# Optimization experiments

Measured on AMD Instinct MI355X. Metric: run time of the kernel, lower is better.

## Reference

```python
import jax, jax.numpy as jnp
import numpy as np
import math

EMBED_DIM = 256
NUM_HEADS = 8
FFN_DIM = 1024
EPS = 1e-5


def layer_norm(x, g, b):
    mu = jnp.mean(x, axis=-1, keepdims=True)
    var = jnp.var(x, axis=-1, keepdims=True)
    return (x - mu) / jnp.sqrt(var + EPS) * g + b


def setup_inputs() -> dict:
    key = jax.random.key(0)
    ks = jax.random.split(key, 10)
    B, L, D, F = 4, 2048, EMBED_DIM, FFN_DIM
    x = jax.random.normal(ks[0], (B, L, D), dtype=jnp.float32)
    mask = jnp.ones((B, L), dtype=jnp.int32)
    # FFN params (PyTorch Linear default-ish scale)
    W1 = jax.random.normal(ks[1], (D, F), dtype=jnp.float32) / np.sqrt(D)
    b1 = jnp.zeros((F,), dtype=jnp.float32)
    W2 = jax.random.normal(ks[2], (F, D), dtype=jnp.float32) / np.sqrt(F)
    b2 = jnp.zeros((D,), dtype=jnp.float32)
    g1 = jnp.ones((D,), dtype=jnp.float32)
    be1 = jnp.zeros((D,), dtype=jnp.float32)
    g2 = jnp.ones((D,), dtype=jnp.float32)
    be2 = jnp.zeros((D,), dtype=jnp.float32)
    return {"x": x, "mask": mask, "W1": W1, "b1": b1, "W2": W2, "b2": b2,
            "g1": g1, "be1": be1, "g2": g2, "be2": be2}


def quantum_attention(x, mask):
    B, L, D = x.shape
    H, dk = NUM_HEADS, D // NUM_HEADS
    xh = x.reshape(B, L, H, dk).transpose(0, 2, 1, 3)  # [B,H,L,dk]
    # per-token mean over batch and heads -> [L, dk]
    m = jnp.mean(xh, axis=(0, 1))
    # closed form of the single-qubit RX circuit: P(|1>) = sin^2(angle/2)
    dot = m @ m.T  # [L, L]
    ang = jnp.clip(dot, -math.pi, math.pi)
    scores = jnp.sin(ang * 0.5) ** 2  # [L, L], shared across B and H
    attn = jnp.broadcast_to(scores[None, None], (B, H, L, L))
    attn = jnp.where(mask[:, None, None, :] == 0, -1e9, attn)
    attn = jax.nn.softmax(attn, axis=-1)
    out = jnp.einsum('bhij,bhjd->bhid', attn, xh)  # values are xh itself
    return out.transpose(0, 2, 1, 3).reshape(B, L, D)


def reference(x, mask, W1, b1, W2, b2, g1, be1, g2, be2):
    attn_out = quantum_attention(x, mask)
    h = layer_norm(x + attn_out, g1, be1)
    ffn = jax.nn.relu(h @ W1 + b1) @ W2 + b2
    return layer_norm(h + ffn, g2, be2)
```

## Files before the change

### kernel.cpp

```cpp
#include <hip/hip_runtime.h>
#include <hip/hip_bf16.h>


#define B_ 4
#define L_ 2048
#define D_ 256
#define F_ 1024
#define PI_F 3.14159265358979323846f

typedef __bf16 bf16x8 __attribute__((ext_vector_type(8)));
typedef float floatx4 __attribute__((ext_vector_type(4)));

__device__ __forceinline__ unsigned short f2bf(float f) {
    unsigned int u = __float_as_uint(f);
    u = (u + 0x7FFFu + ((u >> 16) & 1u)) >> 16;
    return (unsigned short)u;
}
__device__ __forceinline__ float bf2f(unsigned short u) {
    union { unsigned int i; float f; } v; v.i = ((unsigned int)u) << 16; return v.f;
}

__device__ __forceinline__ void async_cp16(unsigned short* lds, const unsigned short* g) {
    __builtin_amdgcn_global_load_lds(
        (const __attribute__((address_space(1))) unsigned int*)g,
        (__attribute__((address_space(3))) unsigned int*)lds, 16, 0, 0);
}

__global__ __launch_bounds__(256) void k_prep(const float* __restrict__ x,
                                              const float* __restrict__ W1,
                                              const float* __restrict__ W2,
                                              const int* __restrict__ mask,
                                              unsigned short* __restrict__ mb,
                                              unsigned short* __restrict__ XmT,
                                              unsigned short* __restrict__ W1T,
                                              unsigned short* __restrict__ W2T) {
    __shared__ float tile[32][33];
    int r = blockIdx.x, t = threadIdx.x;
    if (r >= 2560) {
        if (r < 2816) {
            int idx = (r - 2560) * 256 + t;
            int l = idx >> 5, k = idx & 31;
            float s = 0.f;
#pragma unroll
            for (int b = 0; b < B_; b++) {
                const float* xp = x + ((size_t)(b * L_ + l)) * D_ + k;
#pragma unroll
                for (int h = 0; h < 8; h++) s += xp[h * 32];
            }
            mb[idx] = f2bf(s * (1.f / 32.f));
        } else {
#pragma unroll
            for (int c = 0; c < 32; c++) {
                int e = c * 256 + t;
                int b = e >> 11, j = e & (L_ - 1);
                XmT[(size_t)(1024 + b) * L_ + j] = mask[b * L_ + j] ? 0x3F80 : 0;
            }
        }
        return;
    }
    const float* in; unsigned short* outp; int R, C; const int* mrow = nullptr; size_t bo = 0;
    int bx, by;
    if (r < 2048) {
        int z = r >> 9, rem = r & 511; by = rem >> 3; bx = rem & 7;
        in = x; outp = XmT; R = L_; C = 256; bo = (size_t)z * R * C; mrow = mask + z * L_;
    } else if (r < 2304) {
        int rem = r - 2048; bx = rem & 31; by = rem >> 5;
        in = W1; outp = W1T; R = 256; C = 1024;
    } else {
        int rem = r - 2304; bx = rem & 7; by = rem >> 3;
        in = W2; outp = W2T; R = 1024; C = 256;
    }
    int r0 = by * 32, c0 = bx * 32;
    int tx = t & 31, ty = t >> 5;
#pragma unroll
    for (int rr = 0; rr < 4; rr++) {
        int rw = ty + rr * 8;
        tile[rw][tx] = in[bo + (size_t)(r0 + rw) * C + c0 + tx];
    }
    float mfac = 1.f;
    if (mrow) mfac = mrow[r0 + tx] ? 1.f : 0.f;
    __syncthreads();
#pragma unroll
    for (int rr = 0; rr < 4; rr++) {
        int c = ty + rr * 8;
        outp[bo + (size_t)(c0 + c) * R + r0 + tx] = f2bf(tile[tx][c] * mfac);
    }
}

__global__ __launch_bounds__(256) void k_scores_mfma(const unsigned short* __restrict__ mb,
                                                     unsigned short* __restrict__ E) {
    const int t = threadIdx.x, lane = t & 63, wid = t >> 6;
    const int wm = (wid >> 1) * 64, wn = (wid & 1) * 32;
    const int lr = lane & 15, lq = lane >> 4;
    int m0 = blockIdx.y * 128, n0 = blockIdx.x * 64;
    bf16x8 af[4], bfr[2];
#pragma unroll
    for (int i = 0; i < 4; i++)
        af[i] = *(const bf16x8*)(mb + (size_t)(m0 + wm + i * 16 + lr) * 32 + lq * 8);
#pragma unroll
    for (int j = 0; j < 2; j++)
        bfr[j] = *(const bf16x8*)(mb + (size_t)(n0 + wn + j * 16 + lr) * 32 + lq * 8);
    floatx4 acc[4][2];
#pragma unroll
    for (int i = 0; i < 4; i++)
#pragma unroll
        for (int j = 0; j < 2; j++) {
            acc[i][j] = (floatx4){0.f, 0.f, 0.f, 0.f};
            acc[i][j] = __builtin_amdgcn_mfma_f32_16x16x32_bf16(af[i], bfr[j], acc[i][j], 0, 0, 0);
        }
#pragma unroll
    for (int i = 0; i < 4; i++)
#pragma unroll
        for (int j = 0; j < 2; j++)
#pragma unroll
            for (int r = 0; r < 4; r++) {
                int row = m0 + wm + i * 16 + lq * 4 + r;
                int col = n0 + wn + j * 16 + lr;
                float d = fminf(fmaxf(acc[i][j][r], -PI_F), PI_F);
                float sn = __sinf(0.5f * d);
                E[(size_t)row * L_ + col] = f2bf(__expf(sn * sn));
            }
}

__device__ __forceinline__ void mfma_gemm_async(const unsigned short* __restrict__ A,
                                                const unsigned short* __restrict__ Bt,
                                                int K, int m0, int n0,
                                                unsigned short* sA, unsigned short* sB,
                                                floatx4 acc[4][2]) {
    const int t = threadIdx.x;
    const int lane = t & 63, wid = t >> 6;
    const int wm = (wid >> 1) * 64, wn = (wid & 1) * 32;
    const int lr = lane & 15, lq = lane >> 4;
    const int lrow = lane >> 3, lseg = lane & 7;

    const unsigned short* Ag[4]; unsigned short* sAd[4];
#pragma unroll
    for (int q = 0; q < 4; q++) {
        int rl = wid * 32 + q * 8 + lrow;
        int seg = (lseg - rl) & 7;
        Ag[q] = A + (size_t)(m0 + rl) * K + seg * 8;
        sAd[q] = sA + (wid * 32 + q * 8) * 64;
    }
    const unsigned short* Bg[2]; unsigned short* sBd[2];
#pragma unroll
    for (int q = 0; q < 2; q++) {
        int rl = wid * 16 + q * 8 + lrow;
        int seg = (lseg - rl) & 7;
        Bg[q] = Bt + (size_t)(n0 + rl) * K + seg * 8;
        sBd[q] = sB + (wid * 16 + q * 8) * 64;
    }
    int arot[4], brot[2];
    const unsigned short* sAr[4]; const unsigned short* sBr[2];
#pragma unroll
    for (int i = 0; i < 4; i++) { int ar = wm + i * 16 + lr; sAr[i] = sA + ar * 64; arot[i] = lq + ar; }
#pragma unroll
    for (int j = 0; j < 2; j++) { int br = wn + j * 16 + lr; sBr[j] = sB + br * 64; brot[j] = lq + br; }

    for (int k0 = 0; k0 < K; k0 += 64) {
        __syncthreads();
#pragma unroll
        for (int q = 0; q < 4; q++) async_cp16(sAd[q], Ag[q] + k0);
#pragma unroll
        for (int q = 0; q < 2; q++) async_cp16(sBd[q], Bg[q] + k0);
        __syncthreads();
#pragma unroll
        for (int s = 0; s < 2; s++) {
            bf16x8 af[4], bfr[2];
#pragma unroll
            for (int i = 0; i < 4; i++)
                af[i] = *(const bf16x8*)(sAr[i] + ((s * 4 + arot[i]) & 7) * 8);
#pragma unroll
            for (int j = 0; j < 2; j++)
                bfr[j] = *(const bf16x8*)(sBr[j] + ((s * 4 + brot[j]) & 7) * 8);
#pragma unroll
            for (int i = 0; i < 4; i++)
#pragma unroll
                for (int j = 0; j < 2; j++)
                    acc[i][j] = __builtin_amdgcn_mfma_f32_16x16x32_bf16(af[i], bfr[j], acc[i][j], 0, 0, 0);
        }
    }
}

__global__ __launch_bounds__(256) void k_av(const unsigned short* __restrict__ E,
                                            const unsigned short* __restrict__ XmT,
                                            unsigned short* __restrict__ Cb) {
    __shared__ __align__(16) unsigned short sA[128 * 64];
    __shared__ __align__(16) unsigned short sB[64 * 64];
    floatx4 acc[4][2];
#pragma unroll
    for (int i = 0; i < 4; i++)
#pragma unroll
        for (int j = 0; j < 2; j++) acc[i][j] = (floatx4){0.f, 0.f, 0.f, 0.f};
    int m0 = blockIdx.y * 128, n0 = blockIdx.x * 64;
    mfma_gemm_async(E, XmT, L_, m0, n0, sA, sB, acc);
    const int lane = threadIdx.x & 63, wid = threadIdx.x >> 6;
    const int wm = (wid >> 1) * 64, wn = (wid & 1) * 32;
    const int lr = lane & 15, lq = lane >> 4;
#pragma unroll
    for (int i = 0; i < 4; i++)
#pragma unroll
        for (int j = 0; j < 2; j++)
#pragma unroll
            for (int r = 0; r < 4; r++) {
                int row = m0 + wm + i * 16 + lq * 4 + r;
                int col = n0 + wn + j * 16 + lr;
                Cb[(size_t)row * 1088 + col] = f2bf(acc[i][j][r]);
            }
}

__global__ __launch_bounds__(256) void k_ln1(const float* __restrict__ x, const unsigned short* __restrict__ Cb,
                                             const float* __restrict__ g_, const float* __restrict__ be_,
                                             unsigned short* __restrict__ hb) {
    int tok = blockIdx.x, t = threadIdx.x;
    int b = tok >> 11, i = tok & (L_ - 1);
    float rs = bf2f(Cb[(size_t)i * 1088 + 1024 + b]);
    float v = x[(size_t)tok * D_ + t] + bf2f(Cb[(size_t)i * 1088 + b * 256 + t]) / rs;
    float s = v, s2 = v * v;
    __shared__ float sm[8];
#pragma unroll
    for (int o = 1; o < 64; o <<= 1) { s += __shfl_xor(s, o); s2 += __shfl_xor(s2, o); }
    if ((t & 63) == 0) { sm[t >> 6] = s; sm[4 + (t >> 6)] = s2; }
    __syncthreads();
    s = sm[0] + sm[1] + sm[2] + sm[3];
    s2 = sm[4] + sm[5] + sm[6] + sm[7];
    float mu = s * (1.f / 256.f);
    float var = s2 * (1.f / 256.f) - mu * mu;
    float r = rsqrtf(var + 1e-5f);
    hb[(size_t)tok * D_ + t] = f2bf((v - mu) * r * g_[t] + be_[t]);
}

__global__ __launch_bounds__(256) void k_gemm1(const unsigned short* __restrict__ hb,
                                               const unsigned short* __restrict__ W1T,
                                               const float* __restrict__ b1, unsigned short* __restrict__ t1) {
    __shared__ __align__(16) unsigned short sA[128 * 64];
    __shared__ __align__(16) unsigned short sB[128 * 64];
    const int t = threadIdx.x, lane = t & 63, wid = t >> 6;
    const int wm = (wid >> 1) * 64, wn = (wid & 1) * 64;
    const int lr = lane & 15, lq = lane >> 4;
    const int lrow8 = lane >> 3, lseg = lane & 7;
    int m0 = blockIdx.y * 128, n0 = blockIdx.x * 128;

    const unsigned short* Ag[4]; unsigned short* sAd[4];
    const unsigned short* Bg[4]; unsigned short* sBd[4];
#pragma unroll
    for (int q = 0; q < 4; q++) {
        int rl = q * 32 + wid * 8 + lrow8;
        int seg = (lseg - rl) & 7;
        Ag[q] = hb + (size_t)(m0 + rl) * 256 + seg * 8;
        Bg[q] = W1T + (size_t)(n0 + rl) * 256 + seg * 8;
        sAd[q] = sA + (q * 32 + wid * 8) * 64;
        sBd[q] = sB + (q * 32 + wid * 8) * 64;
    }
    const unsigned short* sAr[4]; int arot[4];
    const unsigned short* sBr[4]; int brot[4];
#pragma unroll
    for (int i = 0; i < 4; i++) { int ar = wm + i * 16 + lr; sAr[i] = sA + ar * 64; arot[i] = lq + ar; }
#pragma unroll
    for (int j = 0; j < 4; j++) { int br = wn + j * 16 + lr; sBr[j] = sB + br * 64; brot[j] = lq + br; }

    floatx4 acc[4][4];
#pragma unroll
    for (int i = 0; i < 4; i++)
#pragma unroll
        for (int j = 0; j < 4; j++) acc[i][j] = (floatx4){0.f, 0.f, 0.f, 0.f};

    for (int k0 = 0; k0 < 256; k0 += 64) {
        __syncthreads();
#pragma unroll
        for (int q = 0; q < 4; q++) { async_cp16(sAd[q], Ag[q] + k0); async_cp16(sBd[q], Bg[q] + k0); }
        __syncthreads();
#pragma unroll
        for (int s = 0; s < 2; s++) {
            bf16x8 af[4], bfr[4];
#pragma unroll
            for (int i = 0; i < 4; i++) af[i] = *(const bf16x8*)(sAr[i] + ((s * 4 + arot[i]) & 7) * 8);
#pragma unroll
            for (int j = 0; j < 4; j++) bfr[j] = *(const bf16x8*)(sBr[j] + ((s * 4 + brot[j]) & 7) * 8);
#pragma unroll
            for (int i = 0; i < 4; i++)
#pragma unroll
                for (int j = 0; j < 4; j++)
                    acc[i][j] = __builtin_amdgcn_mfma_f32_16x16x32_bf16(af[i], bfr[j], acc[i][j], 0, 0, 0);
        }
    }
    float bb[4];
#pragma unroll
    for (int j = 0; j < 4; j++) bb[j] = b1[n0 + wn + j * 16 + lr];
#pragma unroll
    for (int i = 0; i < 4; i++)
#pragma unroll
        for (int j = 0; j < 4; j++) {
            int col = n0 + wn + j * 16 + lr;
#pragma unroll
            for (int r = 0; r < 4; r++) {
                int row = m0 + wm + i * 16 + lq * 4 + r;
                t1[(size_t)row * 1024 + col] = f2bf(fmaxf(acc[i][j][r] + bb[j], 0.f));
            }
        }
}

__global__ __launch_bounds__(256) void k_gemm2ln(const unsigned short* __restrict__ t1,
                                                 const unsigned short* __restrict__ W2T,
                                                 const float* __restrict__ b2,
                                                 const unsigned short* __restrict__ hb,
                                                 const float* __restrict__ g_, const float* __restrict__ be_,
                                                 float* __restrict__ out) {
    __shared__ __align__(16) unsigned short sA[32 * 64];
    __shared__ __align__(16) unsigned short sB[256 * 64];
    __shared__ float red[2][32][2];
    const int t = threadIdx.x, lane = t & 63, wid = t >> 6;
    const int wm = (wid >> 1) * 16, wn = (wid & 1) * 128;
    const int lr = lane & 15, lq = lane >> 4;
    const int lrow8 = lane >> 3, lseg = lane & 7;
    int m0 = blockIdx.x * 32;

    int arl = wid * 8 + lrow8;
    const unsigned short* Ag = t1 + (size_t)(m0 + arl) * 1024 + (((lseg - arl) & 7) * 8);
    unsigned short* sAd = sA + (wid * 8) * 64;
    const unsigned short* Bg[8]; unsigned short* sBd[8];
#pragma unroll
    for (int q = 0; q < 8; q++) {
        int rl = q * 32 + wid * 8 + lrow8;
        Bg[q] = W2T + (size_t)rl * 1024 + (((lseg - rl) & 7) * 8);
        sBd[q] = sB + (q * 32 + wid * 8) * 64;
    }
    const unsigned short* sAr = sA + (wm + lr) * 64; int arot = lq + wm + lr;
    const unsigned short* sBr[8]; int brot[8];
#pragma unroll
    for (int j = 0; j < 8; j++) { int br = wn + j * 16 + lr; sBr[j] = sB + br * 64; brot[j] = lq + br; }

    floatx4 acc[8];
#pragma unroll
    for (int j = 0; j < 8; j++) acc[j] = (floatx4){0.f, 0.f, 0.f, 0.f};

    for (int k0 = 0; k0 < 1024; k0 += 64) {
        __syncthreads();
        async_cp16(sAd, Ag + k0);
#pragma unroll
        for (int q = 0; q < 8; q++) async_cp16(sBd[q], Bg[q] + k0);
        __syncthreads();
#pragma unroll
        for (int s = 0; s < 2; s++) {
            bf16x8 af = *(const bf16x8*)(sAr + ((s * 4 + arot) & 7) * 8);
#pragma unroll
            for (int j = 0; j < 8; j++) {
                bf16x8 bfr = *(const bf16x8*)(sBr[j] + ((s * 4 + brot[j]) & 7) * 8);
                acc[j] = __builtin_amdgcn_mfma_f32_16x16x32_bf16(af, bfr, acc[j], 0, 0, 0);
            }
        }
    }
    float psum[4], psq[4];
#pragma unroll
    for (int r = 0; r < 4; r++) { psum[r] = 0.f; psq[r] = 0.f; }
#pragma unroll
    for (int j = 0; j < 8; j++) {
        int col = wn + j * 16 + lr;
        float bv = b2[col];
#pragma unroll
        for (int r = 0; r < 4; r++) {
            int row = m0 + wm + lq * 4 + r;
            float v = acc[j][r] + bv + bf2f(hb[(size_t)row * 256 + col]);
            acc[j][r] = v;
            psum[r] += v; psq[r] += v * v;
        }
    }
#pragma unroll
    for (int o = 1; o < 16; o <<= 1) {
#pragma unroll
        for (int r = 0; r < 4; r++) { psum[r] += __shfl_xor(psum[r], o); psq[r] += __shfl_xor(psq[r], o); }
    }
    if (lr == 0) {
#pragma unroll
        for (int r = 0; r < 4; r++) {
            int lrow = wm + lq * 4 + r;
            red[wid & 1][lrow][0] = psum[r];
            red[wid & 1][lrow][1] = psq[r];
        }
    }
    __syncthreads();
#pragma unroll
    for (int r = 0; r < 4; r++) {
        int lrow = wm + lq * 4 + r;
        float s = red[0][lrow][0] + red[1][lrow][0];
        float s2 = red[0][lrow][1] + red[1][lrow][1];
        float mu = s * (1.f / 256.f);
        float var = s2 * (1.f / 256.f) - mu * mu;
        float rc = rsqrtf(var + 1e-5f);
        int row = m0 + lrow;
#pragma unroll
        for (int j = 0; j < 8; j++) {
            int col = wn + j * 16 + lr;
            out[(size_t)row * 256 + col] = (acc[j][r] - mu) * rc * g_[col] + be_[col];
        }
    }
}

extern "C" void kernel_launch(void* const* d_in, const int* in_sizes, int n_in,
                              void* d_out, int out_size, void* d_ws, size_t ws_size,
                              hipStream_t stream) {
    const float* x   = (const float*)d_in[0];
    const int*  mask = (const int*)d_in[1];
    const float* W1  = (const float*)d_in[2];
    const float* b1  = (const float*)d_in[3];
    const float* W2  = (const float*)d_in[4];
    const float* b2  = (const float*)d_in[5];
    const float* g1  = (const float*)d_in[6];
    const float* be1 = (const float*)d_in[7];
    const float* g2  = (const float*)d_in[8];
    const float* be2 = (const float*)d_in[9];
    float* out = (float*)d_out;

    char* w = (char*)d_ws;
    unsigned short* mb_   = (unsigned short*)w;  w += 65536 * 2;
    unsigned short* E_    = (unsigned short*)w;  w += (size_t)L_ * L_ * 2;
    unsigned short* XmT_  = (unsigned short*)w;  w += (size_t)1088 * L_ * 2;
    unsigned short* W1T_  = (unsigned short*)w;  w += 262144 * 2;
    unsigned short* W2T_  = (unsigned short*)w;  w += 262144 * 2;
    unsigned short* Cb_   = (unsigned short*)w;  w += (size_t)L_ * 1088 * 2;
    unsigned short* hb_   = (unsigned short*)w;  w += (size_t)8192 * 256 * 2;
    unsigned short* t1_   = (unsigned short*)w;  w += (size_t)8192 * 1024 * 2;

    k_prep<<<2817, 256, 0, stream>>>(x, W1, W2, mask, mb_, XmT_, W1T_, W2T_);
    k_scores_mfma<<<dim3(32, 16), 256, 0, stream>>>(mb_, E_);
    k_av<<<dim3(17, 16), 256, 0, stream>>>(E_, XmT_, Cb_);
    k_ln1<<<B_ * L_, 256, 0, stream>>>(x, Cb_, g1, be1, hb_);
    k_gemm1<<<dim3(8, 64), 256, 0, stream>>>(hb_, W1T_, b1, t1_);
    k_gemm2ln<<<256, 256, 0, stream>>>(t1_, W2T_, b2, hb_, g2, be2, out);
}
```

Before: 150.5 us.

## Double-buffer LDS in GEMM kernels, swizzle block order, vectorize LN1

Converts the k_av, k_gemm1 and k_gemm2ln main loops to a two-stage LDS ping-pong, so the async global-to-LDS copy of the next K slice is issued before computing on the current one. This halves the barriers per step and overlaps load latency with MFMA work, at the cost of doubled shared memory, which may reduce occupancy. Block indices for k_av and k_gemm1 are remapped into a 1D grid with a swizzle to improve L2 reuse. k_ln1 now processes one token per wavefront with float4 loads and no block-level reduction.

```diff
diff --git a/kernel.cpp b/kernel.cpp
--- a/kernel.cpp
+++ b/kernel.cpp
@@ -10,6 +10,7 @@
 
 typedef __bf16 bf16x8 __attribute__((ext_vector_type(8)));
 typedef float floatx4 __attribute__((ext_vector_type(4)));
+typedef unsigned short ushortx4 __attribute__((ext_vector_type(4)));
 
 __device__ __forceinline__ unsigned short f2bf(float f) {
     unsigned int u = __float_as_uint(f);
@@ -122,80 +123,80 @@
             }
 }
 
-__device__ __forceinline__ void mfma_gemm_async(const unsigned short* __restrict__ A,
-                                                const unsigned short* __restrict__ Bt,
-                                                int K, int m0, int n0,
-                                                unsigned short* sA, unsigned short* sB,
-                                                floatx4 acc[4][2]) {
-    const int t = threadIdx.x;
-    const int lane = t & 63, wid = t >> 6;
+__global__ __launch_bounds__(256) void k_av(const unsigned short* __restrict__ E,
+                                            const unsigned short* __restrict__ XmT,
+                                            unsigned short* __restrict__ Cb) {
+    __shared__ __align__(16) unsigned short sA[2][128 * 64];
+    __shared__ __align__(16) unsigned short sB[2][64 * 64];
+    const int t = threadIdx.x, lane = t & 63, wid = t >> 6;
     const int wm = (wid >> 1) * 64, wn = (wid & 1) * 32;
     const int lr = lane & 15, lq = lane >> 4;
     const int lrow = lane >> 3, lseg = lane & 7;
 
-    const unsigned short* Ag[4]; unsigned short* sAd[4];
+    int bid = blockIdx.x;
+    int swz = (bid & 7) * 34 + (bid >> 3);
+    int m0 = (swz / 17) * 128, n0 = (swz % 17) * 64;
+
+    const unsigned short* Ag[4]; int sAoff[4];
 #pragma unroll
     for (int q = 0; q < 4; q++) {
         int rl = wid * 32 + q * 8 + lrow;
-        int seg = (lseg - rl) & 7;
-        Ag[q] = A + (size_t)(m0 + rl) * K + seg * 8;
-        sAd[q] = sA + (wid * 32 + q * 8) * 64;
-    }
-    const unsigned short* Bg[2]; unsigned short* sBd[2];
+        Ag[q] = E + (size_t)(m0 + rl) * L_ + ((lseg - rl) & 7) * 8;
+        sAoff[q] = (wid * 32 + q * 8) * 64;
+    }
+    const unsigned short* Bg[2]; int sBoff[2];
 #pragma unroll
     for (int q = 0; q < 2; q++) {
         int rl = wid * 16 + q * 8 + lrow;
-        int seg = (lseg - rl) & 7;
-        Bg[q] = Bt + (size_t)(n0 + rl) * K + seg * 8;
-        sBd[q] = sB + (wid * 16 + q * 8) * 64;
-    }
-    int arot[4], brot[2];
-    const unsigned short* sAr[4]; const unsigned short* sBr[2];
-#pragma unroll
-    for (int i = 0; i < 4; i++) { int ar = wm + i * 16 + lr; sAr[i] = sA + ar * 64; arot[i] = lq + ar; }
-#pragma unroll
-    for (int j = 0; j < 2; j++) { int br = wn + j * 16 + lr; sBr[j] = sB + br * 64; brot[j] = lq + br; }
-
-    for (int k0 = 0; k0 < K; k0 += 64) {
-        __syncthreads();
-#pragma unroll
-        for (int q = 0; q < 4; q++) async_cp16(sAd[q], Ag[q] + k0);
-#pragma unroll
-        for (int q = 0; q < 2; q++) async_cp16(sBd[q], Bg[q] + k0);
-        __syncthreads();
+        Bg[q] = XmT + (size_t)(n0 + rl) * L_ + ((lseg - rl) & 7) * 8;
+        sBoff[q] = (wid * 16 + q * 8) * 64;
+    }
+    int arot[4], aroff[4], brot[2], broff[2];
+#pragma unroll
+    for (int i = 0; i < 4; i++) { int ar = wm + i * 16 + lr; aroff[i] = ar * 64; arot[i] = lq + ar; }
+#pragma unroll
+    for (int j = 0; j < 2; j++) { int br = wn + j * 16 + lr; broff[j] = br * 64; brot[j] = lq + br; }
+
+    floatx4 acc[4][2];
+#pragma unroll
+    for (int i = 0; i < 4; i++)
+#pragma unroll
+        for (int j = 0; j < 2; j++) acc[i][j] = (floatx4){0.f, 0.f, 0.f, 0.f};
+
+    auto stage = [&](unsigned short* dA, unsigned short* dB, int k0) {
+#pragma unroll
+        for (int q = 0; q < 4; q++) async_cp16(dA + sAoff[q], Ag[q] + k0);
+#pragma unroll
+        for (int q = 0; q < 2; q++) async_cp16(dB + sBoff[q], Bg[q] + k0);
+    };
+    auto compute = [&](const unsigned short* cA, const unsigned short* cB) {
 #pragma unroll
         for (int s = 0; s < 2; s++) {
             bf16x8 af[4], bfr[2];
 #pragma unroll
             for (int i = 0; i < 4; i++)
-                af[i] = *(const bf16x8*)(sAr[i] + ((s * 4 + arot[i]) & 7) * 8);
+                af[i] = *(const bf16x8*)(cA + aroff[i] + ((s * 4 + arot[i]) & 7) * 8);
 #pragma unroll
             for (int j = 0; j < 2; j++)
-                bfr[j] = *(const bf16x8*)(sBr[j] + ((s * 4 + brot[j]) & 7) * 8);
+                bfr[j] = *(const bf16x8*)(cB + broff[j] + ((s * 4 + brot[j]) & 7) * 8);
 #pragma unroll
             for (int i = 0; i < 4; i++)
 #pragma unroll
                 for (int j = 0; j < 2; j++)
                     acc[i][j] = __builtin_amdgcn_mfma_f32_16x16x32_bf16(af[i], bfr[j], acc[i][j], 0, 0, 0);
         }
-    }
-}
-
-__global__ __launch_bounds__(256) void k_av(const unsigned short* __restrict__ E,
-                                            const unsigned short* __restrict__ XmT,
-                                            unsigned short* __restrict__ Cb) {
-    __shared__ __align__(16) unsigned short sA[128 * 64];
-    __shared__ __align__(16) unsigned short sB[64 * 64];
-    floatx4 acc[4][2];
-#pragma unroll
-    for (int i = 0; i < 4; i++)
-#pragma unroll
-        for (int j = 0; j < 2; j++) acc[i][j] = (floatx4){0.f, 0.f, 0.f, 0.f};
-    int m0 = blockIdx.y * 128, n0 = blockIdx.x * 64;
-    mfma_gemm_async(E, XmT, L_, m0, n0, sA, sB, acc);
-    const int lane = threadIdx.x & 63, wid = threadIdx.x >> 6;
-    const int wm = (wid >> 1) * 64, wn = (wid & 1) * 32;
-    const int lr = lane & 15, lq = lane >> 4;
+    };
+
+    stage(sA[0], sB[0], 0);
+    __syncthreads();
+    for (int st = 0; st < 32; st += 2) {
+        stage(sA[1], sB[1], (st + 1) << 6);
+        compute(sA[0], sB[0]);
+        __syncthreads();
+        if (st + 2 < 32) stage(sA[0], sB[0], (st + 2) << 6);
+        compute(sA[1], sB[1]);
+        __syncthreads();
+    }
 #pragma unroll
     for (int i = 0; i < 4; i++)
 #pragma unroll
@@ -211,52 +212,61 @@
 __global__ __launch_bounds__(256) void k_ln1(const float* __restrict__ x, const unsigned short* __restrict__ Cb,
                                              const float* __restrict__ g_, const float* __restrict__ be_,
                                              unsigned short* __restrict__ hb) {
-    int tok = blockIdx.x, t = threadIdx.x;
+    int t = threadIdx.x, wid = t >> 6, lane = t & 63;
+    int tok = (blockIdx.x << 2) + wid;
     int b = tok >> 11, i = tok & (L_ - 1);
     float rs = bf2f(Cb[(size_t)i * 1088 + 1024 + b]);
-    float v = x[(size_t)tok * D_ + t] + bf2f(Cb[(size_t)i * 1088 + b * 256 + t]) / rs;
-    float s = v, s2 = v * v;
-    __shared__ float sm[8];
+    float4 xv = *(const float4*)(x + (size_t)tok * D_ + lane * 4);
+    ushortx4 cv = *(const ushortx4*)(Cb + (size_t)i * 1088 + b * 256 + lane * 4);
+    float v0 = xv.x + bf2f(cv.x) / rs;
+    float v1 = xv.y + bf2f(cv.y) / rs;
+    float v2 = xv.z + bf2f(cv.z) / rs;
+    float v3 = xv.w + bf2f(cv.w) / rs;
+    float s  = v0 + v1 + v2 + v3;
+    float s2 = v0 * v0 + v1 * v1 + v2 * v2 + v3 * v3;
 #pragma unroll
     for (int o = 1; o < 64; o <<= 1) { s += __shfl_xor(s, o); s2 += __shfl_xor(s2, o); }
-    if ((t & 63) == 0) { sm[t >> 6] = s; sm[4 + (t >> 6)] = s2; }
-    __syncthreads();
-    s = sm[0] + sm[1] + sm[2] + sm[3];
-    s2 = sm[4] + sm[5] + sm[6] + sm[7];
     float mu = s * (1.f / 256.f);
     float var = s2 * (1.f / 256.f) - mu * mu;
     float r = rsqrtf(var + 1e-5f);
-    hb[(size_t)tok * D_ + t] = f2bf((v - mu) * r * g_[t] + be_[t]);
+    float4 gv = *(const float4*)(g_ + lane * 4);
+    float4 bv = *(const float4*)(be_ + lane * 4);
+    ushortx4 o4;
+    o4.x = f2bf((v0 - mu) * r * gv.x + bv.x);
+    o4.y = f2bf((v1 - mu) * r * gv.y + bv.y);
+    o4.z = f2bf((v2 - mu) * r * gv.z + bv.z);
+    o4.w = f2bf((v3 - mu) * r * gv.w + bv.w);
+    *(ushortx4*)(hb + (size_t)tok * D_ + lane * 4) = o4;
 }
 
 __global__ __launch_bounds__(256) void k_gemm1(const unsigned short* __restrict__ hb,
                                                const unsigned short* __restrict__ W1T,
                                                const float* __restrict__ b1, unsigned short* __restrict__ t1) {
-    __shared__ __align__(16) unsigned short sA[128 * 64];
-    __shared__ __align__(16) unsigned short sB[128 * 64];
+    __shared__ __align__(16) unsigned short sA[2][128 * 64];
+    __shared__ __align__(16) unsigned short sB[2][128 * 64];
     const int t = threadIdx.x, lane = t & 63, wid = t >> 6;
     const int wm = (wid >> 1) * 64, wn = (wid & 1) * 64;
     const int lr = lane & 15, lq = lane >> 4;
     const int lrow8 = lane >> 3, lseg = lane & 7;
-    int m0 = blockIdx.y * 128, n0 = blockIdx.x * 128;
-
-    const unsigned short* Ag[4]; unsigned short* sAd[4];
-    const unsigned short* Bg[4]; unsigned short* sBd[4];
+
+    int bid = blockIdx.x;
+    int swz = (bid & 7) * 64 + (bid >> 3);
+    int m0 = (swz >> 3) * 128, n0 = (swz & 7) * 128;
+
+    const unsigned short* Ag[4]; const unsigned short* Bg[4]; int soff[4];
 #pragma unroll
     for (int q = 0; q < 4; q++) {
         int rl = q * 32 + wid * 8 + lrow8;
         int seg = (lseg - rl) & 7;
         Ag[q] = hb + (size_t)(m0 + rl) * 256 + seg * 8;
         Bg[q] = W1T + (size_t)(n0 + rl) * 256 + seg * 8;
-        sAd[q] = sA + (q * 32 + wid * 8) * 64;
-        sBd[q] = sB + (q * 32 + wid * 8) * 64;
-    }
-    const unsigned short* sAr[4]; int arot[4];
-    const unsigned short* sBr[4]; int brot[4];
-#pragma unroll
-    for (int i = 0; i < 4; i++) { int ar = wm + i * 16 + lr; sAr[i] = sA + ar * 64; arot[i] = lq + ar; }
-#pragma unroll
-    for (int j = 0; j < 4; j++) { int br = wn + j * 16 + lr; sBr[j] = sB + br * 64; brot[j] = lq + br; }
+        soff[q] = (q * 32 + wid * 8) * 64;
+    }
+    int arot[4], aroff[4], brot[4], broff[4];
+#pragma unroll
+    for (int i = 0; i < 4; i++) { int ar = wm + i * 16 + lr; aroff[i] = ar * 64; arot[i] = lq + ar; }
+#pragma unroll
+    for (int j = 0; j < 4; j++) { int br = wn + j * 16 + lr; broff[j] = br * 64; brot[j] = lq + br; }
 
     floatx4 acc[4][4];
 #pragma unroll
@@ -264,24 +274,35 @@
 #pragma unroll
         for (int j = 0; j < 4; j++) acc[i][j] = (floatx4){0.f, 0.f, 0.f, 0.f};
 
-    for (int k0 = 0; k0 < 256; k0 += 64) {
-        __syncthreads();
-#pragma unroll
-        for (int q = 0; q < 4; q++) { async_cp16(sAd[q], Ag[q] + k0); async_cp16(sBd[q], Bg[q] + k0); }
-        __syncthreads();
+    auto stage = [&](unsigned short* dA, unsigned short* dB, int k0) {
+#pragma unroll
+        for (int q = 0; q < 4; q++) { async_cp16(dA + soff[q], Ag[q] + k0); async_cp16(dB + soff[q], Bg[q] + k0); }
+    };
+    auto compute = [&](const unsigned short* cA, const unsigned short* cB) {
 #pragma unroll
         for (int s = 0; s < 2; s++) {
             bf16x8 af[4], bfr[4];
 #pragma unroll
-            for (int i = 0; i < 4; i++) af[i] = *(const bf16x8*)(sAr[i] + ((s * 4 + arot[i]) & 7) * 8);
-#pragma unroll
-            for (int j = 0; j < 4; j++) bfr[j] = *(const bf16x8*)(sBr[j] + ((s * 4 + brot[j]) & 7) * 8);
+            for (int i = 0; i < 4; i++) af[i] = *(const bf16x8*)(cA + aroff[i] + ((s * 4 + arot[i]) & 7) * 8);
+#pragma unroll
+            for (int j = 0; j < 4; j++) bfr[j] = *(const bf16x8*)(cB + broff[j] + ((s * 4 + brot[j]) & 7) * 8);
 #pragma unroll
             for (int i = 0; i < 4; i++)
 #pragma unroll
                 for (int j = 0; j < 4; j++)
                     acc[i][j] = __builtin_amdgcn_mfma_f32_16x16x32_bf16(af[i], bfr[j], acc[i][j], 0, 0, 0);
         }
+    };
+
+    stage(sA[0], sB[0], 0);
+    __syncthreads();
+    for (int st = 0; st < 4; st += 2) {
+        stage(sA[1], sB[1], (st + 1) << 6);
+        compute(sA[0], sB[0]);
+        __syncthreads();
+        if (st + 2 < 4) stage(sA[0], sB[0], (st + 2) << 6);
+        compute(sA[1], sB[1]);
+        __syncthreads();
     }
     float bb[4];
 #pragma unroll
@@ -305,8 +326,8 @@
                                                  const unsigned short* __restrict__ hb,
                                                  const float* __restrict__ g_, const float* __restrict__ be_,
                                                  float* __restrict__ out) {
-    __shared__ __align__(16) unsigned short sA[32 * 64];
-    __shared__ __align__(16) unsigned short sB[256 * 64];
+    __shared__ __align__(16) unsigned short sA[2][32 * 64];
+    __shared__ __align__(16) unsigned short sB[2][256 * 64];
     __shared__ float red[2][32][2];
     const int t = threadIdx.x, lane = t & 63, wid = t >> 6;
     const int wm = (wid >> 1) * 16, wn = (wid & 1) * 128;
@@ -316,38 +337,49 @@
 
     int arl = wid * 8 + lrow8;
     const unsigned short* Ag = t1 + (size_t)(m0 + arl) * 1024 + (((lseg - arl) & 7) * 8);
-    unsigned short* sAd = sA + (wid * 8) * 64;
-    const unsigned short* Bg[8]; unsigned short* sBd[8];
+    int sAoff = (wid * 8) * 64;
+    const unsigned short* Bg[8]; int sBoff[8];
 #pragma unroll
     for (int q = 0; q < 8; q++) {
         int rl = q * 32 + wid * 8 + lrow8;
         Bg[q] = W2T + (size_t)rl * 1024 + (((lseg - rl) & 7) * 8);
-        sBd[q] = sB + (q * 32 + wid * 8) * 64;
-    }
-    const unsigned short* sAr = sA + (wm + lr) * 64; int arot = lq + wm + lr;
-    const unsigned short* sBr[8]; int brot[8];
-#pragma unroll
-    for (int j = 0; j < 8; j++) { int br = wn + j * 16 + lr; sBr[j] = sB + br * 64; brot[j] = lq + br; }
+        sBoff[q] = (q * 32 + wid * 8) * 64;
+    }
+    int aroff = (wm + lr) * 64, arot = lq + wm + lr;
+    int brot[8], broff[8];
+#pragma unroll
+    for (int j = 0; j < 8; j++) { int br = wn + j * 16 + lr; broff[j] = br * 64; brot[j] = lq + br; }
 
     floatx4 acc[8];
 #pragma unroll
     for (int j = 0; j < 8; j++) acc[j] = (floatx4){0.f, 0.f, 0.f, 0.f};
 
-    for (int k0 = 0; k0 < 1024; k0 += 64) {
-        __syncthreads();
-        async_cp16(sAd, Ag + k0);
-#pragma unroll
-        for (int q = 0; q < 8; q++) async_cp16(sBd[q], Bg[q] + k0);
-        __syncthreads();
+    auto stage = [&](unsigned short* dA, unsigned short* dB, int k0) {
+        async_cp16(dA + sAoff, Ag + k0);
+#pragma unroll
+        for (int q = 0; q < 8; q++) async_cp16(dB + sBoff[q], Bg[q] + k0);
+    };
+    auto compute = [&](const unsigned short* cA, const unsigned short* cB) {
 #pragma unroll
         for (int s = 0; s < 2; s++) {
-            bf16x8 af = *(const bf16x8*)(sAr + ((s * 4 + arot) & 7) * 8);
+            bf16x8 af = *(const bf16x8*)(cA + aroff + ((s * 4 + arot) & 7) * 8);
 #pragma unroll
             for (int j = 0; j < 8; j++) {
-                bf16x8 bfr = *(const bf16x8*)(sBr[j] + ((s * 4 + brot[j]) & 7) * 8);
+                bf16x8 bfr = *(const bf16x8*)(cB + broff[j] + ((s * 4 + brot[j]) & 7) * 8);
                 acc[j] = __builtin_amdgcn_mfma_f32_16x16x32_bf16(af, bfr, acc[j], 0, 0, 0);
             }
         }
+    };
+
+    stage(sA[0], sB[0], 0);
+    __syncthreads();
+    for (int st = 0; st < 16; st += 2) {
+        stage(sA[1], sB[1], (st + 1) << 6);
+        compute(sA[0], sB[0]);
+        __syncthreads();
+        if (st + 2 < 16) stage(sA[0], sB[0], (st + 2) << 6);
+        compute(sA[1], sB[1]);
+        __syncthreads();
     }
     float psum[4], psq[4];
 #pragma unroll
@@ -422,8 +454,8 @@
 
     k_prep<<<2817, 256, 0, stream>>>(x, W1, W2, mask, mb_, XmT_, W1T_, W2T_);
     k_scores_mfma<<<dim3(32, 16), 256, 0, stream>>>(mb_, E_);
-    k_av<<<dim3(17, 16), 256, 0, stream>>>(E_, XmT_, Cb_);
-    k_ln1<<<B_ * L_, 256, 0, stream>>>(x, Cb_, g1, be1, hb_);
-    k_gemm1<<<dim3(8, 64), 256, 0, stream>>>(hb_, W1T_, b1, t1_);
+    k_av<<<272, 256, 0, stream>>>(E_, XmT_, Cb_);
+    k_ln1<<<2048, 256, 0, stream>>>(x, Cb_, g1, be1, hb_);
+    k_gemm1<<<512, 256, 0, stream>>>(hb_, W1T_, b1, t1_);
     k_gemm2ln<<<256, 256, 0, stream>>>(t1_, W2T_, b2, hb_, g2, be2, out);
 }
```

After: 149.2 us. No clear change (-0.8%).
